# Kernel optimization log

Hardware: AMD Instinct MI355X
Metric: run time of the kernel (lower is better)

Reference implementation:

```python
import jax, jax.numpy as jnp
import numpy as np

N_LEVELS = 16
LOG2_T = 19
T = 1 << LOG2_T
BASE = 16
MAXRES = 4096
F = 2
MAXC = 16  # (max_SH_degree+1)^2
PER_LEVEL_SCALE = float(np.exp((np.log(MAXRES) - np.log(BASE)) / (N_LEVELS - 1)))
RES = jnp.asarray([BASE * PER_LEVEL_SCALE ** l for l in range(N_LEVELS)], dtype=jnp.float32)
PRIMES = jnp.array([1, 2654435761, 805459861], dtype=jnp.uint32)
OFFS = jnp.asarray([[(i >> 2) & 1, (i >> 1) & 1, i & 1] for i in range(8)], dtype=jnp.int32)  # (8,3)

C0 = 0.28209479177387814
C1 = 0.4886025119029199
C2 = (1.0925484305920792, -1.0925484305920792, 0.31539156525252005, -1.0925484305920792, 0.5462742152960396)
C3 = (-0.5900435899266435, 2.890611442640554, -0.4570457994644658, 0.3731763325901154, -0.4570457994644658, 1.445305721320277, -0.5900435899266435)


def hash_encode(x, table):
    # x: (N,3) in [0,1]; table: (L,T,F). Multiresolution hash grid (tcnn HashGrid).
    def level(tab, res):
        p = x * res
        p0 = jnp.floor(p)
        w = p - p0                                  # (N,3) trilerp weights
        c = p0.astype(jnp.uint32)[:, None, :] + OFFS[None].astype(jnp.uint32)  # (N,8,3)
        h = (c[..., 0] * PRIMES[0]) ^ (c[..., 1] * PRIMES[1]) ^ (c[..., 2] * PRIMES[2])
        idx = (h & jnp.uint32(T - 1)).astype(jnp.int32)
        f = tab[idx]                                # (N,8,F) irregular gather
        wc = jnp.where(OFFS[None].astype(bool), w[:, None, :], 1.0 - w[:, None, :]).prod(-1)
        return (f * wc[..., None]).sum(1)           # (N,F)
    feats = jax.vmap(level)(table, RES)             # (L,N,F)
    return feats.transpose(1, 0, 2).reshape(x.shape[0], N_LEVELS * F)


def sh_basis(d):
    # real SH basis up to degree 3; d: (N,3) unit vectors -> (N,16)
    x, y, z = d[..., 0], d[..., 1], d[..., 2]
    xx, yy, zz = x * x, y * y, z * z
    xy, yz, xz = x * y, y * z, x * z
    return jnp.stack([
        jnp.full_like(x, C0), -C1 * y, C1 * z, -C1 * x,
        C2[0] * xy, C2[1] * yz, C2[2] * (2 * zz - xx - yy), C2[3] * xz, C2[4] * (xx - yy),
        C3[0] * y * (3 * xx - yy), C3[1] * xy * z, C3[2] * y * (4 * zz - xx - yy),
        C3[3] * z * (2 * zz - 3 * xx - 3 * yy), C3[4] * x * (4 * zz - xx - yy),
        C3[5] * z * (xx - yy), C3[6] * x * (xx - 3 * yy)], axis=-1)


def network_forward(positions, rx_pos, table, W1, W2, aabb, active_deg):
    aabb_min, aabb_max = aabb[:3], aabb[3:]
    scale = jnp.maximum(aabb_max - aabb_min, 1e-6)
    norm_pos = (positions - aabb_min) / scale
    selector = jnp.all((norm_pos >= 0.0) & (norm_pos <= 1.0), axis=-1)  # (N,)
    pos_n = jnp.clip(norm_pos, 0.0, 1.0)  # safe values for masked-out points (zeroed below)

    def density_fn(pn):
        feats = hash_encode(pn, table)
        h = jax.nn.relu(feats @ W1)
        sh = (h @ W2).reshape(-1, MAXC, 2)
        dens = C0 * sh[:, 0, :]                     # (N,2) = (real, imag) of sigma
        return jnp.sqrt(dens[:, 0] ** 2 + dens[:, 1] ** 2).sum(), (dens, sh)

    # in-forward autograd: grad of sum |sigma| w.r.t. normalized positions
    (_, (dens, sh)), g = jax.value_and_grad(density_fn, has_aux=True)(pos_n)
    g_world = g / scale
    nrm = -g_world / jnp.maximum(jnp.linalg.norm(g_world, axis=-1, keepdims=True), 1e-20)
    nrm = jnp.where(jnp.isnan(nrm), 0.0, nrm)

    # EvalSH: view direction from sample point toward receiver, SH dot coefficients
    dirs = rx_pos - positions
    dirs = dirs / jnp.maximum(jnp.linalg.norm(dirs, axis=-1, keepdims=True), 1e-20)
    Y = sh_basis(dirs)                              # (N,16)
    mask = (jnp.arange(MAXC) < (active_deg + 1) ** 2).astype(Y.dtype)
    scat = jnp.einsum('nc,ncf->nf', Y * mask, sh)   # (N,2) complex as (re,im)

    sel = selector[:, None]
    dens = jnp.where(sel, dens, 0.0)
    scat = jnp.where(sel, scat, 0.0)
    nrm = jnp.where(sel, nrm, 0.0)
    shz = jnp.where(selector[:, None, None], sh, 0.0)
    # pack: sigma(re,im) | scatterers_to(re,im) | normals(3) | sh_coeffs(32) -> (N,39)
    return jnp.concatenate([dens, scat, nrm, shz.reshape(-1, MAXC * 2)], axis=-1)


def setup_inputs() -> dict:
    key = jax.random.key(0)
    ks = jax.random.split(key, 6)
    N = 262144
    positions = jax.random.uniform(ks[0], (N, 3), jnp.float32) * 2.2 - 1.1
    rx_pos = jax.random.normal(ks[1], (3,), jnp.float32) * 2.0
    table = (jax.random.uniform(ks[2], (N_LEVELS, T, F), jnp.float32) * 2.0 - 1.0) * 1e-4
    d_in, hid, d_out = N_LEVELS * F, 32, MAXC * 2
    W1 = jax.random.normal(ks[3], (d_in, hid), jnp.float32) / np.sqrt(d_in)
    W2 = jax.random.normal(ks[4], (hid, d_out), jnp.float32) / np.sqrt(hid)
    aabb = jnp.array([-1.0, -1.0, -1.0, 1.0, 1.0, 1.0], jnp.float32)
    return {"positions": positions, "rx_pos": rx_pos, "table": table, "W1": W1,
            "W2": W2, "aabb": aabb, "active_deg": 3}


def reference(positions, rx_pos, table, W1, W2, aabb, active_deg):
    return network_forward(positions, rx_pos, table, W1, W2, aabb, active_deg)
```

## Files before the change

### kernel.cpp

```cpp
#include <hip/hip_runtime.h>
#include <cmath>

#pragma clang fp contract(off)

#define NLV 16
#define TSZ (1u << 19)
#define TMASK (TSZ - 1u)
#define PR1 2654435761u
#define PR2 805459861u

struct ResT { float r[NLV]; };

__global__ __launch_bounds__(256, 2) void ngp_fused(
    const float* __restrict__ g_pos,
    const float* __restrict__ g_rx,
    const float* __restrict__ g_tab,
    const float* __restrict__ g_W1,
    const float* __restrict__ g_W2,
    const float* __restrict__ g_aabb,
    const int*   __restrict__ g_deg,
    float* __restrict__ g_out,
    int N, ResT rt)
{
    __shared__ float sm[48][256];

    int tid = blockIdx.x * 256 + threadIdx.x;
    int lt  = threadIdx.x;
    int n = tid >> 1;
    int p = tid & 1;
    if (n >= N) return;

    float a0 = g_aabb[0], a1 = g_aabb[1], a2 = g_aabb[2];
    float s0 = fmaxf(g_aabb[3] - a0, 1e-6f);
    float s1 = fmaxf(g_aabb[4] - a1, 1e-6f);
    float s2 = fmaxf(g_aabb[5] - a2, 1e-6f);
    float posx = g_pos[3*n+0], posy = g_pos[3*n+1], posz = g_pos[3*n+2];
    float nx = (posx - a0) / s0;
    float ny = (posy - a1) / s1;
    float nz = (posz - a2) / s2;
    bool sel = (nx >= 0.f) && (nx <= 1.f) && (ny >= 0.f) && (ny <= 1.f)
            && (nz >= 0.f) && (nz <= 1.f);
    float pnx = fminf(fmaxf(nx, 0.f), 1.f);
    float pny = fminf(fmaxf(ny, 0.f), 1.f);
    float pnz = fminf(fmaxf(nz, 0.f), 1.f);

    const float2* tab = (const float2*)g_tab;

    float f0o[8], f1o[8];
#pragma unroll
    for (int j = 0; j < 8; ++j) {
        float res = p ? rt.r[8+j] : rt.r[j];
        const float2* tl = tab + (size_t)(p * 8 + j) * TSZ;
        float fx = pnx * res, fy = pny * res, fz = pnz * res;
        float x0 = floorf(fx), y0 = floorf(fy), z0 = floorf(fz);
        float wx = fx - x0, wy = fy - y0, wz = fz - z0;
        float omx = 1.f - wx, omy = 1.f - wy, omz = 1.f - wz;
        unsigned ux = (unsigned)x0, uy = (unsigned)y0, uz = (unsigned)z0;
        unsigned hx0 = ux,        hx1 = ux + 1u;
        unsigned hy0 = uy * PR1,  hy1 = (uy + 1u) * PR1;
        unsigned hz0 = uz * PR2,  hz1 = (uz + 1u) * PR2;
        float f0 = 0.f, f1 = 0.f;
        float lxa = 0.f, lxb = 0.f, lya = 0.f, lyb = 0.f, lza = 0.f, lzb = 0.f;
#pragma unroll
        for (int c = 0; c < 8; ++c) {
            unsigned hh = ((c & 4) ? hx1 : hx0) ^ ((c & 2) ? hy1 : hy0) ^ ((c & 1) ? hz1 : hz0);
            float2 fv = tl[hh & TMASK];
            float wxv = (c & 4) ? wx : omx;
            float wyv = (c & 2) ? wy : omy;
            float wzv = (c & 1) ? wz : omz;
            float wgt = wxv * wyv;
            wgt = wgt * wzv;
            float t0 = fv.x * wgt;
            float t1 = fv.y * wgt;
            f0 = f0 + t0;
            f1 = f1 + t1;
            float pyz = wyv * wzv;
            float pxz = wxv * wzv;
            float pxy = wxv * wyv;
            float spx = (c & 4) ? pyz : -pyz;
            float spy = (c & 2) ? pxz : -pxz;
            float spz = (c & 1) ? pxy : -pxy;
            lxa = lxa + fv.x * spx;  lxb = lxb + fv.y * spx;
            lya = lya + fv.x * spy;  lyb = lyb + fv.y * spy;
            lza = lza + fv.x * spz;  lzb = lzb + fv.y * spz;
        }
        f0o[j] = f0; f1o[j] = f1;
        sm[j*6+0][lt] = lxa;  sm[j*6+1][lt] = lxb;
        sm[j*6+2][lt] = lya;  sm[j*6+3][lt] = lyb;
        sm[j*6+4][lt] = lza;  sm[j*6+5][lt] = lzb;
    }

    float z1[32];
#pragma unroll
    for (int i = 0; i < 32; ++i) z1[i] = 0.f;

    float hi0[8], hi1[8];
#pragma unroll
    for (int j = 0; j < 8; ++j) {
        float t0 = __shfl_xor(f0o[j], 1, 64);
        float t1 = __shfl_xor(f1o[j], 1, 64);
        float lo0 = p ? t0 : f0o[j];
        float lo1 = p ? t1 : f1o[j];
        hi0[j] = p ? f0o[j] : t0;
        hi1[j] = p ? f1o[j] : t1;
        const float* w1a = g_W1 + (2*j) * 32;
        const float* w1b = g_W1 + (2*j+1) * 32;
#pragma unroll
        for (int i = 0; i < 32; ++i) {
            float acc = fmaf(lo0, w1a[i], z1[i]);
            z1[i] = fmaf(lo1, w1b[i], acc);
        }
    }
#pragma unroll
    for (int j = 0; j < 8; ++j) {
        const float* w1a = g_W1 + (2*(8+j)) * 32;
        const float* w1b = g_W1 + (2*(8+j)+1) * 32;
#pragma unroll
        for (int i = 0; i < 32; ++i) {
            float acc = fmaf(hi0[j], w1a[i], z1[i]);
            z1[i] = fmaf(hi1[j], w1b[i], acc);
        }
    }

    unsigned mask = 0u;
    float sh[32];
#pragma unroll
    for (int o = 0; o < 32; ++o) sh[o] = 0.f;
#pragma unroll
    for (int i = 0; i < 32; ++i) {
        bool on = (z1[i] > 0.f);
        if (on) mask |= (1u << i);
        float h = on ? z1[i] : 0.f;
        const float* w2r = g_W2 + i * 32;
#pragma unroll
        for (int o = 0; o < 32; ++o) sh[o] = fmaf(h, w2r[o], sh[o]);
    }

    const float C0c = 0.28209479177387814f;
    float d0 = C0c * sh[0], d1 = C0c * sh[1];

    float rx0 = g_rx[0], rx1 = g_rx[1], rx2 = g_rx[2];
    float dxw = rx0 - posx, dyw = rx1 - posy, dzw = rx2 - posz;
    float dnorm = sqrtf(dxw*dxw + dyw*dyw + dzw*dzw);
    float dinv = 1.f / fmaxf(dnorm, 1e-20f);
    float X = dxw * dinv, Yd = dyw * dinv, Z = dzw * dinv;
    float xx = X*X, yy = Yd*Yd, zz = Z*Z;
    float xy = X*Yd, yz = Yd*Z, xz = X*Z;
    float Yb[16];
    Yb[0]  = 0.28209479177387814f;
    Yb[1]  = -0.4886025119029199f * Yd;
    Yb[2]  =  0.4886025119029199f * Z;
    Yb[3]  = -0.4886025119029199f * X;
    Yb[4]  =  1.0925484305920792f * xy;
    Yb[5]  = -1.0925484305920792f * yz;
    Yb[6]  =  0.31539156525252005f * (2.f*zz - xx - yy);
    Yb[7]  = -1.0925484305920792f * xz;
    Yb[8]  =  0.5462742152960396f * (xx - yy);
    Yb[9]  = -0.5900435899266435f * Yd * (3.f*xx - yy);
    Yb[10] =  2.890611442640554f  * xy * Z;
    Yb[11] = -0.4570457994644658f * Yd * (4.f*zz - xx - yy);
    Yb[12] =  0.3731763325901154f * Z * (2.f*zz - 3.f*xx - 3.f*yy);
    Yb[13] = -0.4570457994644658f * X * (4.f*zz - xx - yy);
    Yb[14] =  1.445305721320277f  * Z * (xx - yy);
    Yb[15] = -0.5900435899266435f * X * (xx - 3.f*yy);

    int deg = g_deg[0];
    int nact = (deg + 1) * (deg + 1);
    float sc0 = 0.f, sc1 = 0.f;
#pragma unroll
    for (int c = 0; c < 16; ++c) {
        float yc = (c < nact) ? Yb[c] : 0.f;
        sc0 = fmaf(yc, sh[2*c+0], sc0);
        sc1 = fmaf(yc, sh[2*c+1], sc1);
    }

    float* op = g_out + (size_t)n * 39;
    if (p == 0) {
        op[0] = sel ? d0  : 0.f;
        op[1] = sel ? d1  : 0.f;
        op[2] = sel ? sc0 : 0.f;
        op[3] = sel ? sc1 : 0.f;
#pragma unroll
        for (int c = 0; c < 13; ++c) op[7 + c] = sel ? sh[c] : 0.f;
    } else {
#pragma unroll
        for (int c = 13; c < 32; ++c) op[7 + c] = sel ? sh[c] : 0.f;
    }

    float ss = d0*d0 + d1*d1;
    float q0 = 0.f, q1 = 0.f;
    if (ss > 0.f) {
        float sr = sqrtf(ss);
        q0 = C0c * d0 / sr;
        q1 = C0c * d1 / sr;
    }
    float dzv[32];
#pragma unroll
    for (int i = 0; i < 32; ++i) {
        float dh = fmaf(q0, g_W2[i*32+0], q1 * g_W2[i*32+1]);
        dzv[i] = ((mask >> i) & 1u) ? dh : 0.f;
    }

    float gx = 0.f, gy = 0.f, gz = 0.f;
    const float4* w1v = (const float4*)g_W1;
    int rbase = p * 16;
#pragma unroll
    for (int j = 0; j < 8; ++j) {
        const float4* wa = w1v + (size_t)(rbase + 2*j) * 8;
        const float4* wb = wa + 8;
        float da = 0.f, db = 0.f;
#pragma unroll
        for (int k = 0; k < 8; ++k) {
            float4 va = wa[k], vb = wb[k];
            da = fmaf(va.x, dzv[4*k+0], da);
            da = fmaf(va.y, dzv[4*k+1], da);
            da = fmaf(va.z, dzv[4*k+2], da);
            da = fmaf(va.w, dzv[4*k+3], da);
            db = fmaf(vb.x, dzv[4*k+0], db);
            db = fmaf(vb.y, dzv[4*k+1], db);
            db = fmaf(vb.z, dzv[4*k+2], db);
            db = fmaf(vb.w, dzv[4*k+3], db);
        }
        float xa = sm[j*6+0][lt], xb = sm[j*6+1][lt];
        float ya = sm[j*6+2][lt], yb = sm[j*6+3][lt];
        float za = sm[j*6+4][lt], zb = sm[j*6+5][lt];
        float res = p ? rt.r[8+j] : rt.r[j];
        gx = fmaf(res, fmaf(da, xa, db * xb), gx);
        gy = fmaf(res, fmaf(da, ya, db * yb), gy);
        gz = fmaf(res, fmaf(da, za, db * zb), gz);
    }
    float tx = __shfl_xor(gx, 1, 64);
    float ty = __shfl_xor(gy, 1, 64);
    float tz = __shfl_xor(gz, 1, 64);
    gx = gx + tx; gy = gy + ty; gz = gz + tz;

    float gwx = gx / s0, gwy = gy / s1, gwz = gz / s2;
    float gn = sqrtf(gwx*gwx + gwy*gwy + gwz*gwz);
    float ginv = -1.f / fmaxf(gn, 1e-20f);
    if (p == 0) {
        op[4] = sel ? gwx * ginv : 0.f;
        op[5] = sel ? gwy * ginv : 0.f;
        op[6] = sel ? gwz * ginv : 0.f;
    }
}

extern "C" void kernel_launch(void* const* d_in, const int* in_sizes, int n_in,
                              void* d_out, int out_size, void* d_ws, size_t ws_size,
                              hipStream_t stream)
{
    const float* g_pos  = (const float*)d_in[0];
    const float* g_rx   = (const float*)d_in[1];
    const float* g_tab  = (const float*)d_in[2];
    const float* g_W1   = (const float*)d_in[3];
    const float* g_W2   = (const float*)d_in[4];
    const float* g_aabb = (const float*)d_in[5];
    const int*   g_deg  = (const int*)d_in[6];
    float* g_out = (float*)d_out;

    int N = in_sizes[0] / 3;

    ResT rt;
    double scale = exp((log(4096.0) - log(16.0)) / 15.0);
    for (int l = 0; l < NLV; ++l) rt.r[l] = (float)(16.0 * pow(scale, (double)l));

    long long threads = 2LL * N;
    int blocks = (int)((threads + 255) / 256);
    ngp_fused<<<blocks, 256, 0, stream>>>(g_pos, g_rx, g_tab, g_W1, g_W2,
                                          g_aabb, g_deg, g_out, N, rt);
}
```

Baseline: 406.4 us.

## Split fused hash-grid kernel into per-level gather and MLP/backward passes

Adds a two-kernel path: one kernel computes each level's trilinear hash features and spatial-derivative partials per point into a workspace, and a second kernel runs the MLP, SH evaluation and normal backward pass from those buffers. This is meant to shrink per-thread register pressure and raise the parallelism available to the random table gathers. In exchange it writes and re-reads a large intermediate buffer in global memory. The old fused kernel stays as a fallback when the workspace is too small.

```diff
diff --git a/kernel.cpp b/kernel.cpp
--- a/kernel.cpp
+++ b/kernel.cpp
@@ -10,6 +10,244 @@
 #define PR2 805459861u
 
 struct ResT { float r[NLV]; };
+
+__device__ __forceinline__ void aabb_norm(
+    const float* __restrict__ g_aabb, float posx, float posy, float posz,
+    float& s0, float& s1, float& s2,
+    float& pnx, float& pny, float& pnz, bool& sel)
+{
+    float a0 = g_aabb[0], a1 = g_aabb[1], a2 = g_aabb[2];
+    s0 = fmaxf(g_aabb[3] - a0, 1e-6f);
+    s1 = fmaxf(g_aabb[4] - a1, 1e-6f);
+    s2 = fmaxf(g_aabb[5] - a2, 1e-6f);
+    float nx = (posx - a0) / s0;
+    float ny = (posy - a1) / s1;
+    float nz = (posz - a2) / s2;
+    sel = (nx >= 0.f) && (nx <= 1.f) && (ny >= 0.f) && (ny <= 1.f)
+       && (nz >= 0.f) && (nz <= 1.f);
+    pnx = fminf(fmaxf(nx, 0.f), 1.f);
+    pny = fminf(fmaxf(ny, 0.f), 1.f);
+    pnz = fminf(fmaxf(nz, 0.f), 1.f);
+}
+
+__global__ __launch_bounds__(256) void level_gather(
+    const float* __restrict__ g_pos,
+    const float* __restrict__ g_tab,
+    const float* __restrict__ g_aabb,
+    float* __restrict__ ws,
+    int N, ResT rt)
+{
+    int b = blockIdx.x;
+    int lvl = b & 15;
+    int n = (b >> 4) * 256 + threadIdx.x;
+    if (n >= N) return;
+
+    float posx = g_pos[3*n+0], posy = g_pos[3*n+1], posz = g_pos[3*n+2];
+    float s0, s1, s2, pnx, pny, pnz; bool sel;
+    aabb_norm(g_aabb, posx, posy, posz, s0, s1, s2, pnx, pny, pnz, sel);
+
+    float res = rt.r[lvl];
+    const float2* tl = (const float2*)g_tab + (size_t)lvl * TSZ;
+
+    float fx = pnx * res, fy = pny * res, fz = pnz * res;
+    float x0 = floorf(fx), y0 = floorf(fy), z0 = floorf(fz);
+    float wx = fx - x0, wy = fy - y0, wz = fz - z0;
+    float omx = 1.f - wx, omy = 1.f - wy, omz = 1.f - wz;
+    unsigned ux = (unsigned)x0, uy = (unsigned)y0, uz = (unsigned)z0;
+    unsigned hx0 = ux,        hx1 = ux + 1u;
+    unsigned hy0 = uy * PR1,  hy1 = (uy + 1u) * PR1;
+    unsigned hz0 = uz * PR2,  hz1 = (uz + 1u) * PR2;
+    float f0 = 0.f, f1 = 0.f;
+    float lxa = 0.f, lxb = 0.f, lya = 0.f, lyb = 0.f, lza = 0.f, lzb = 0.f;
+#pragma unroll
+    for (int c = 0; c < 8; ++c) {
+        unsigned hh = ((c & 4) ? hx1 : hx0) ^ ((c & 2) ? hy1 : hy0) ^ ((c & 1) ? hz1 : hz0);
+        float2 fv = tl[hh & TMASK];
+        float wxv = (c & 4) ? wx : omx;
+        float wyv = (c & 2) ? wy : omy;
+        float wzv = (c & 1) ? wz : omz;
+        float wgt = wxv * wyv;
+        wgt = wgt * wzv;
+        float t0 = fv.x * wgt;
+        float t1 = fv.y * wgt;
+        f0 = f0 + t0;
+        f1 = f1 + t1;
+        float pyz = wyv * wzv;
+        float pxz = wxv * wzv;
+        float pxy = wxv * wyv;
+        float spx = (c & 4) ? pyz : -pyz;
+        float spy = (c & 2) ? pxz : -pxz;
+        float spz = (c & 1) ? pxy : -pxy;
+        lxa = lxa + fv.x * spx;  lxb = lxb + fv.y * spx;
+        lya = lya + fv.x * spy;  lyb = lyb + fv.y * spy;
+        lza = lza + fv.x * spz;  lzb = lzb + fv.y * spz;
+    }
+
+    size_t LN = (size_t)NLV * N;
+    size_t base = (size_t)lvl * N + n;
+    ws[0*LN + base] = f0;
+    ws[1*LN + base] = f1;
+    ws[2*LN + base] = lxa;
+    ws[3*LN + base] = lxb;
+    ws[4*LN + base] = lya;
+    ws[5*LN + base] = lyb;
+    ws[6*LN + base] = lza;
+    ws[7*LN + base] = lzb;
+}
+
+__global__ __launch_bounds__(256) void mlp_bwd(
+    const float* __restrict__ g_pos,
+    const float* __restrict__ g_rx,
+    const float* __restrict__ g_W1,
+    const float* __restrict__ g_W2,
+    const float* __restrict__ g_aabb,
+    const int*   __restrict__ g_deg,
+    const float* __restrict__ ws,
+    float* __restrict__ g_out,
+    int N, ResT rt)
+{
+    int n = blockIdx.x * 256 + threadIdx.x;
+    if (n >= N) return;
+
+    float posx = g_pos[3*n+0], posy = g_pos[3*n+1], posz = g_pos[3*n+2];
+    float s0, s1, s2, pnx, pny, pnz; bool sel;
+    aabb_norm(g_aabb, posx, posy, posz, s0, s1, s2, pnx, pny, pnz, sel);
+    (void)pnx; (void)pny; (void)pnz;
+
+    size_t LN = (size_t)NLV * N;
+    const float* f0w = ws + 0*LN;
+    const float* f1w = ws + 1*LN;
+
+    float z1[32];
+#pragma unroll
+    for (int i = 0; i < 32; ++i) z1[i] = 0.f;
+    for (int l = 0; l < NLV; ++l) {
+        float f0 = f0w[(size_t)l * N + n];
+        float f1 = f1w[(size_t)l * N + n];
+        const float* w1a = g_W1 + (2*l) * 32;
+        const float* w1b = g_W1 + (2*l+1) * 32;
+#pragma unroll
+        for (int i = 0; i < 32; ++i) {
+            float acc = fmaf(f0, w1a[i], z1[i]);
+            z1[i] = fmaf(f1, w1b[i], acc);
+        }
+    }
+
+    unsigned mask = 0u;
+    float sh[32];
+#pragma unroll
+    for (int o = 0; o < 32; ++o) sh[o] = 0.f;
+#pragma unroll
+    for (int i = 0; i < 32; ++i) {
+        bool on = (z1[i] > 0.f);
+        if (on) mask |= (1u << i);
+        float h = on ? z1[i] : 0.f;
+        const float* w2r = g_W2 + i * 32;
+#pragma unroll
+        for (int o = 0; o < 32; ++o) sh[o] = fmaf(h, w2r[o], sh[o]);
+    }
+
+    const float C0c = 0.28209479177387814f;
+    float d0 = C0c * sh[0], d1 = C0c * sh[1];
+
+    float rx0 = g_rx[0], rx1 = g_rx[1], rx2 = g_rx[2];
+    float dxw = rx0 - posx, dyw = rx1 - posy, dzw = rx2 - posz;
+    float dnorm = sqrtf(dxw*dxw + dyw*dyw + dzw*dzw);
+    float dinv = 1.f / fmaxf(dnorm, 1e-20f);
+    float X = dxw * dinv, Yd = dyw * dinv, Z = dzw * dinv;
+    float xx = X*X, yy = Yd*Yd, zz = Z*Z;
+    float xy = X*Yd, yz = Yd*Z, xz = X*Z;
+    float Yb[16];
+    Yb[0]  = 0.28209479177387814f;
+    Yb[1]  = -0.4886025119029199f * Yd;
+    Yb[2]  =  0.4886025119029199f * Z;
+    Yb[3]  = -0.4886025119029199f * X;
+    Yb[4]  =  1.0925484305920792f * xy;
+    Yb[5]  = -1.0925484305920792f * yz;
+    Yb[6]  =  0.31539156525252005f * (2.f*zz - xx - yy);
+    Yb[7]  = -1.0925484305920792f * xz;
+    Yb[8]  =  0.5462742152960396f * (xx - yy);
+    Yb[9]  = -0.5900435899266435f * Yd * (3.f*xx - yy);
+    Yb[10] =  2.890611442640554f  * xy * Z;
+    Yb[11] = -0.4570457994644658f * Yd * (4.f*zz - xx - yy);
+    Yb[12] =  0.3731763325901154f * Z * (2.f*zz - 3.f*xx - 3.f*yy);
+    Yb[13] = -0.4570457994644658f * X * (4.f*zz - xx - yy);
+    Yb[14] =  1.445305721320277f  * Z * (xx - yy);
+    Yb[15] = -0.5900435899266435f * X * (xx - 3.f*yy);
+
+    int deg = g_deg[0];
+    int nact = (deg + 1) * (deg + 1);
+    float sc0 = 0.f, sc1 = 0.f;
+#pragma unroll
+    for (int c = 0; c < 16; ++c) {
+        float yc = (c < nact) ? Yb[c] : 0.f;
+        sc0 = fmaf(yc, sh[2*c+0], sc0);
+        sc1 = fmaf(yc, sh[2*c+1], sc1);
+    }
+
+    float* op = g_out + (size_t)n * 39;
+    op[0] = sel ? d0  : 0.f;
+    op[1] = sel ? d1  : 0.f;
+    op[2] = sel ? sc0 : 0.f;
+    op[3] = sel ? sc1 : 0.f;
+#pragma unroll
+    for (int c = 0; c < 32; ++c) op[7 + c] = sel ? sh[c] : 0.f;
+
+    float ss = d0*d0 + d1*d1;
+    float q0 = 0.f, q1 = 0.f;
+    if (ss > 0.f) {
+        float sr = sqrtf(ss);
+        q0 = C0c * d0 / sr;
+        q1 = C0c * d1 / sr;
+    }
+    float dzv[32];
+#pragma unroll
+    for (int i = 0; i < 32; ++i) {
+        float dh = fmaf(q0, g_W2[i*32+0], q1 * g_W2[i*32+1]);
+        dzv[i] = ((mask >> i) & 1u) ? dh : 0.f;
+    }
+
+    const float* mxaw = ws + 2*LN;
+    const float* mxbw = ws + 3*LN;
+    const float* myaw = ws + 4*LN;
+    const float* mybw = ws + 5*LN;
+    const float* mzaw = ws + 6*LN;
+    const float* mzbw = ws + 7*LN;
+    float gx = 0.f, gy = 0.f, gz = 0.f;
+    const float4* w1v = (const float4*)g_W1;
+    for (int l = 0; l < NLV; ++l) {
+        const float4* wa = w1v + (size_t)(2*l) * 8;
+        const float4* wb = wa + 8;
+        float da = 0.f, db = 0.f;
+#pragma unroll
+        for (int k = 0; k < 8; ++k) {
+            float4 va = wa[k], vb = wb[k];
+            da = fmaf(va.x, dzv[4*k+0], da);
+            da = fmaf(va.y, dzv[4*k+1], da);
+            da = fmaf(va.z, dzv[4*k+2], da);
+            da = fmaf(va.w, dzv[4*k+3], da);
+            db = fmaf(vb.x, dzv[4*k+0], db);
+            db = fmaf(vb.y, dzv[4*k+1], db);
+            db = fmaf(vb.z, dzv[4*k+2], db);
+            db = fmaf(vb.w, dzv[4*k+3], db);
+        }
+        size_t base = (size_t)l * N + n;
+        float xa = mxaw[base], xb = mxbw[base];
+        float ya = myaw[base], yb = mybw[base];
+        float za = mzaw[base], zb = mzbw[base];
+        float res = rt.r[l];
+        gx = fmaf(res, fmaf(da, xa, db * xb), gx);
+        gy = fmaf(res, fmaf(da, ya, db * yb), gy);
+        gz = fmaf(res, fmaf(da, za, db * zb), gz);
+    }
+
+    float gwx = gx / s0, gwy = gy / s1, gwz = gz / s2;
+    float gn = sqrtf(gwx*gwx + gwy*gwy + gwz*gwz);
+    float ginv = -1.f / fmaxf(gn, 1e-20f);
+    op[4] = sel ? gwx * ginv : 0.f;
+    op[5] = sel ? gwy * ginv : 0.f;
+    op[6] = sel ? gwz * ginv : 0.f;
+}
 
 __global__ __launch_bounds__(256, 2) void ngp_fused(
     const float* __restrict__ g_pos,
@@ -30,22 +268,11 @@
     int p = tid & 1;
     if (n >= N) return;
 
-    float a0 = g_aabb[0], a1 = g_aabb[1], a2 = g_aabb[2];
-    float s0 = fmaxf(g_aabb[3] - a0, 1e-6f);
-    float s1 = fmaxf(g_aabb[4] - a1, 1e-6f);
-    float s2 = fmaxf(g_aabb[5] - a2, 1e-6f);
     float posx = g_pos[3*n+0], posy = g_pos[3*n+1], posz = g_pos[3*n+2];
-    float nx = (posx - a0) / s0;
-    float ny = (posy - a1) / s1;
-    float nz = (posz - a2) / s2;
-    bool sel = (nx >= 0.f) && (nx <= 1.f) && (ny >= 0.f) && (ny <= 1.f)
-            && (nz >= 0.f) && (nz <= 1.f);
-    float pnx = fminf(fmaxf(nx, 0.f), 1.f);
-    float pny = fminf(fmaxf(ny, 0.f), 1.f);
-    float pnz = fminf(fmaxf(nz, 0.f), 1.f);
+    float s0, s1, s2, pnx, pny, pnz; bool sel;
+    aabb_norm(g_aabb, posx, posy, posz, s0, s1, s2, pnx, pny, pnz, sel);
 
     const float2* tab = (const float2*)g_tab;
-
     float f0o[8], f1o[8];
 #pragma unroll
     for (int j = 0; j < 8; ++j) {
@@ -93,7 +320,6 @@
     float z1[32];
 #pragma unroll
     for (int i = 0; i < 32; ++i) z1[i] = 0.f;
-
     float hi0[8], hi1[8];
 #pragma unroll
     for (int j = 0; j < 8; ++j) {
@@ -263,8 +489,18 @@
     double scale = exp((log(4096.0) - log(16.0)) / 15.0);
     for (int l = 0; l < NLV; ++l) rt.r[l] = (float)(16.0 * pow(scale, (double)l));
 
-    long long threads = 2LL * N;
-    int blocks = (int)((threads + 255) / 256);
-    ngp_fused<<<blocks, 256, 0, stream>>>(g_pos, g_rx, g_tab, g_W1, g_W2,
-                                          g_aabb, g_deg, g_out, N, rt);
+    size_t need = (size_t)NLV * N * 8 * sizeof(float);
+    if (ws_size >= need) {
+        float* ws = (float*)d_ws;
+        int chunks = (N + 255) / 256;
+        level_gather<<<NLV * chunks, 256, 0, stream>>>(g_pos, g_tab, g_aabb,
+                                                       ws, N, rt);
+        mlp_bwd<<<chunks, 256, 0, stream>>>(g_pos, g_rx, g_W1, g_W2, g_aabb,
+                                            g_deg, ws, g_out, N, rt);
+    } else {
+        long long threads = 2LL * N;
+        int blocks = (int)((threads + 255) / 256);
+        ngp_fused<<<blocks, 256, 0, stream>>>(g_pos, g_rx, g_tab, g_W1, g_W2,
+                                              g_aabb, g_deg, g_out, N, rt);
+    }
 }
```

After: 360.9 us. -11.2%, faster.
